# Optimization experiments

Hardware: AMD Instinct MI355X
Metric: run time of the kernel (lower is better)

## Reference

```python
import jax, jax.numpy as jnp
import numpy as np

N, R, E, DIN, DOUT, B = 40000, 16, 50000, 256, 256, 4


def setup_inputs() -> dict:
    key = jax.random.key(0)
    ks = jax.random.split(key, 7)
    xav = (2.0 / (DIN + DOUT)) ** 0.5  # xavier-ish scale
    x = jax.random.normal(ks[0], (N, DIN), jnp.float32)
    bases = jax.random.normal(ks[1], (B, DIN, DOUT), jnp.float32) * xav
    coeff = jax.random.normal(ks[2], (R, B), jnp.float32) * 0.5
    loop_weight = jax.random.normal(ks[3], (DIN, DOUT), jnp.float32) * xav
    h_bias = jnp.zeros((DOUT,), jnp.float32)
    edge_src = jax.random.randint(ks[4], (R, E), 0, N, dtype=jnp.int64)
    edge_dst = jax.random.randint(ks[5], (R, E), 0, N, dtype=jnp.int64)
    return {"x": x, "bases": bases, "coeff": coeff, "loop_weight": loop_weight,
            "h_bias": h_bias, "edge_src": edge_src, "edge_dst": edge_dst}


def reference(x, bases, coeff, loop_weight, h_bias, edge_src, edge_dst):
    # Basis decomposition: per-relation weight W_r = sum_b coeff[r,b] * bases[b]
    W = jnp.einsum('rb,bio->rio', coeff, bases)  # [R, DIN, DOUT]
    n = x.shape[0]

    def body(acc, rel):
        W_r, src, dst = rel
        # transform all nodes once, gather at edge sources
        m = (x @ W_r)[src]                                   # [E, DOUT]
        agg = jax.ops.segment_sum(m, dst, num_segments=n)    # [N, DOUT]
        deg = jax.ops.segment_sum(jnp.ones(src.shape, jnp.float32), dst,
                                  num_segments=n)            # in-degree per rel
        # norm='right': divide by dst in-degree (clamped to 1)
        return acc + agg / jnp.clip(deg, 1.0)[:, None], None

    h0 = jnp.zeros((n, loop_weight.shape[1]), x.dtype)
    h, _ = jax.lax.scan(body, h0, (W, edge_src, edge_dst))   # sum over relations
    h = h + x @ loop_weight + h_bias                         # self-loop + bias
    return jax.nn.relu(h)
```

## Files before the change

### kernel.cpp

```cpp
#include <hip/hip_runtime.h>
#include <stdint.h>

#define NN   40000
#define RR   16
#define EE   50000
#define DD   256
#define NB   4
#define KTOT (NB*DD + DD)
#define BM   128
#define BN   128
#define BK   32
#define NITER (KTOT/BK)

#define SCAN_BLK  40
#define SCAN_ELEM 1024

typedef __bf16 bf16x8 __attribute__((ext_vector_type(8)));
typedef float  f32x4  __attribute__((ext_vector_type(4)));
typedef float  f32x2  __attribute__((ext_vector_type(2)));
typedef unsigned short ushort_t;

__device__ inline unsigned short f2bf(float f) {
    unsigned int b = __builtin_bit_cast(unsigned int, f);
    b += 0x7FFFu + ((b >> 16) & 1u);
    return (unsigned short)(b >> 16);
}

__device__ __forceinline__ void gll16(const void* g, void* l) {
    __builtin_amdgcn_global_load_lds(
        (__attribute__((address_space(1))) void*)(uintptr_t)g,
        (__attribute__((address_space(3))) void*)(uint32_t)(uintptr_t)l,
        16, 0, 0);
}


#define CAST_BLKS ((NN * DD / 4 + DD * KTOT + 255) / 256)
#define DEG_BLKS  ((RR * EE + 255) / 256)

__global__ __launch_bounds__(256) void k_prep(const float* __restrict__ x,
                                              const float* __restrict__ bases,
                                              const float* __restrict__ lw,
                                              const int* __restrict__ edst,
                                              ushort_t* __restrict__ xb,
                                              ushort_t* __restrict__ Bt,
                                              int* __restrict__ deg) {
    int b = blockIdx.x;
    if (b < CAST_BLKS) {
        int t = b * 256 + threadIdx.x;
        const int NX = NN * DD / 4;
        if (t < NX) {
            float4 f = *(const float4*)(x + (size_t)t * 4);
            ushort4 o;
            o.x = f2bf(f.x); o.y = f2bf(f.y); o.z = f2bf(f.z); o.w = f2bf(f.w);
            *(ushort4*)(xb + (size_t)t * 4) = o;
        } else {
            int u = t - NX;
            if (u < DD * KTOT) {
                int o = u / KTOT, k = u - o * KTOT;
                float f = (k < NB * DD) ? bases[(size_t)k * DD + o]
                                        : lw[(size_t)(k - NB * DD) * DD + o];
                Bt[u] = f2bf(f);
            }
        }
    } else {
        int e = (b - CAST_BLKS) * 256 + threadIdx.x;
        if (e < RR * EE) {
            int r = e / EE;
            atomicAdd(&deg[r * NN + edst[e]], 1);
        }
    }
}

__global__ __launch_bounds__(256) void k_scanA(const int* __restrict__ deg,
                                               int* __restrict__ offsets,
                                               int* __restrict__ bsum) {
    __shared__ int part[256];
    int t = threadIdx.x, b = blockIdx.x;
    int g = b * SCAN_ELEM + t * 4;
    int4 h = {0, 0, 0, 0};
    if (g < NN) {
#pragma unroll
        for (int r = 0; r < RR; r++) {
            int4 d = *(const int4*)(deg + (size_t)r * NN + g);
            h.x += d.x; h.y += d.y; h.z += d.z; h.w += d.w;
        }
    }
    int s = h.x + h.y + h.z + h.w;
    part[t] = s;
    __syncthreads();
    for (int off = 1; off < 256; off <<= 1) {
        int v = (t >= off) ? part[t - off] : 0;
        __syncthreads();
        part[t] += v;
        __syncthreads();
    }
    int ex = part[t] - s;
    if (g < NN) {
        int4 o;
        o.x = ex;
        o.y = ex + h.x;
        o.z = ex + h.x + h.y;
        o.w = ex + h.x + h.y + h.z;
        *(int4*)(offsets + g) = o;
    }
    if (t == 255) bsum[b] = part[255];
}

__global__ __launch_bounds__(256) void k_scanB(const int* __restrict__ bsum,
                                               int* __restrict__ offsets,
                                               int* __restrict__ cursor) {
    __shared__ int sbase, stot;
    int t = threadIdx.x, b = blockIdx.x;
    if (t == 0) {
        int acc = 0, base = 0;
        for (int i = 0; i < SCAN_BLK; i++) {
            if (i == b) base = acc;
            acc += bsum[i];
        }
        sbase = base;
        stot = acc;
    }
    __syncthreads();
    int base = sbase;
    int g = b * SCAN_ELEM + t * 4;
    if (g < NN) {
        int4 o = *(const int4*)(offsets + g);
        o.x += base; o.y += base; o.z += base; o.w += base;
        *(int4*)(offsets + g) = o;
        *(int4*)(cursor + g) = o;
    }
    if (b == SCAN_BLK - 1 && t == 0) offsets[NN] = stot;
}

__global__ __launch_bounds__(256) void k_escatter(const int* __restrict__ esrc,
                                                  const int* __restrict__ edst,
                                                  int* __restrict__ cursor,
                                                  unsigned int* __restrict__ recs) {
    int e = blockIdx.x * blockDim.x + threadIdx.x;
    if (e >= RR * EE) return;
    int r = e / EE;
    int d = edst[e];
    int pos = atomicAdd(&cursor[d], 1);
    recs[pos] = (unsigned int)esrc[e] | ((unsigned int)r << 16);
}

__global__ __launch_bounds__(256) void k_gather(const ushort_t* __restrict__ xb,
                                                const float* __restrict__ coeff,
                                                const int* __restrict__ deg,
                                                const int* __restrict__ offsets,
                                                const unsigned int* __restrict__ recs,
                                                ushort_t* __restrict__ vb) {
    __shared__ float wtab[4][64];
    int lane = threadIdx.x & 63;
    int wv   = threadIdx.x >> 6;
    int n    = __builtin_amdgcn_readfirstlane(blockIdx.x * 4 + wv);

    {
        int r  = lane >> 2;
        int dg = deg[r * NN + n];
        float inv = 1.0f / (float)(dg > 0 ? dg : 1);
        wtab[wv][lane] = coeff[lane] * inv;
    }

    int beg = offsets[n], end = offsets[n + 1];
    f32x2 a[4][2];
#pragma unroll
    for (int b = 0; b < 4; b++) { a[b][0] = (f32x2){0,0}; a[b][1] = (f32x2){0,0}; }

    const float* wrow = &wtab[wv][0];
    const ushort_t* xl = xb + lane * 4;

    auto acc_edge = [&](uint2 u, float4 w) {
        f32x2 lo, hi;
        lo.x = __builtin_bit_cast(float, u.x << 16);
        lo.y = __builtin_bit_cast(float, u.x & 0xFFFF0000u);
        hi.x = __builtin_bit_cast(float, u.y << 16);
        hi.y = __builtin_bit_cast(float, u.y & 0xFFFF0000u);
        a[0][0] = lo * (f32x2){w.x, w.x} + a[0][0];
        a[0][1] = hi * (f32x2){w.x, w.x} + a[0][1];
        a[1][0] = lo * (f32x2){w.y, w.y} + a[1][0];
        a[1][1] = hi * (f32x2){w.y, w.y} + a[1][1];
        a[2][0] = lo * (f32x2){w.z, w.z} + a[2][0];
        a[2][1] = hi * (f32x2){w.z, w.z} + a[2][1];
        a[3][0] = lo * (f32x2){w.w, w.w} + a[3][0];
        a[3][1] = hi * (f32x2){w.w, w.w} + a[3][1];
    };

    int ei = beg;
    for (; ei + 4 <= end; ei += 4) {
        unsigned int r0 = recs[ei + 0];
        unsigned int r1 = recs[ei + 1];
        unsigned int r2 = recs[ei + 2];
        unsigned int r3 = recs[ei + 3];
        uint2 u0 = *(const uint2*)(xl + (size_t)(r0 & 0xFFFFu) * DD);
        uint2 u1 = *(const uint2*)(xl + (size_t)(r1 & 0xFFFFu) * DD);
        uint2 u2 = *(const uint2*)(xl + (size_t)(r2 & 0xFFFFu) * DD);
        uint2 u3 = *(const uint2*)(xl + (size_t)(r3 & 0xFFFFu) * DD);
        float4 w0 = *(const float4*)&wrow[(r0 >> 16) * 4];
        float4 w1 = *(const float4*)&wrow[(r1 >> 16) * 4];
        float4 w2 = *(const float4*)&wrow[(r2 >> 16) * 4];
        float4 w3 = *(const float4*)&wrow[(r3 >> 16) * 4];
        acc_edge(u0, w0);
        acc_edge(u1, w1);
        acc_edge(u2, w2);
        acc_edge(u3, w3);
    }
    for (; ei < end; ei++) {
        unsigned int r0 = recs[ei];
        uint2 u0 = *(const uint2*)(xl + (size_t)(r0 & 0xFFFFu) * DD);
        float4 w0 = *(const float4*)&wrow[(r0 >> 16) * 4];
        acc_edge(u0, w0);
    }

    ushort_t* vr = vb + (size_t)n * (NB * DD) + lane * 4;
#pragma unroll
    for (int b = 0; b < 4; b++) {
        ushort4 o;
        o.x = f2bf(a[b][0].x); o.y = f2bf(a[b][0].y);
        o.z = f2bf(a[b][1].x); o.w = f2bf(a[b][1].y);
        *(ushort4*)(vr + b * DD) = o;
    }
}

__global__ __launch_bounds__(256) void k_gemm(const ushort_t* __restrict__ vb,
                                              const ushort_t* __restrict__ xb,
                                              const ushort_t* __restrict__ Bt,
                                              const float* __restrict__ bias,
                                              float* __restrict__ out) {
    __shared__ __align__(16) ushort_t As[2][BM * BK];
    __shared__ __align__(16) ushort_t Bs[2][BN * BK];
    int tid  = threadIdx.x;
    int lane = tid & 63;
    int w    = tid >> 6;
    int wr   = w >> 1, wc = w & 1;
    int rowbase = blockIdx.y * BM;
    int nbase   = blockIdx.x * BN;
    int ml = lane & 15, q = lane >> 4;

    int srow  = tid >> 2;
    int g     = (tid & 3) ^ ((tid >> 4) & 3);
    int wbase = __builtin_amdgcn_readfirstlane(w << 10);

    int arow0 = rowbase + srow;       if (arow0 >= NN) arow0 = NN - 1;
    int arow1 = rowbase + 64 + srow;  if (arow1 >= NN) arow1 = NN - 1;
    const ushort_t* pvA0 = vb + (size_t)arow0 * (NB * DD) + g * 8;
    const ushort_t* pvA1 = vb + (size_t)arow1 * (NB * DD) + g * 8;
    const ushort_t* pxA0 = xb + (size_t)arow0 * DD + g * 8;
    const ushort_t* pxA1 = xb + (size_t)arow1 * DD + g * 8;
    const ushort_t* pB0  = Bt + (size_t)(nbase + srow) * KTOT + g * 8;
    const ushort_t* pB1  = Bt + (size_t)(nbase + 64 + srow) * KTOT + g * 8;

    f32x4 acc[4][4];
#pragma unroll
    for (int i = 0; i < 4; i++)
#pragma unroll
        for (int j = 0; j < 4; j++) acc[i][j] = (f32x4){0, 0, 0, 0};

    int aoff[4], boff[4];
#pragma unroll
    for (int i = 0; i < 4; i++) {
        int m = wr * 64 + i * 16 + ml;
        aoff[i] = m * BK + ((q ^ ((m >> 2) & 3)) * 8);
    }
#pragma unroll
    for (int j = 0; j < 4; j++) {
        int n = wc * 64 + j * 16 + ml;
        boff[j] = n * BK + ((q ^ ((n >> 2) & 3)) * 8);
    }

    auto stage = [&](int s, int kb) {
        const ushort_t* a0 = (kb < NB * DD) ? pvA0 + kb : pxA0 + (kb - NB * DD);
        const ushort_t* a1 = (kb < NB * DD) ? pvA1 + kb : pxA1 + (kb - NB * DD);
        char* ab = (char*)&As[s][0] + wbase;
        char* bb = (char*)&Bs[s][0] + wbase;
        gll16(a0,       ab);
        gll16(a1,       ab + 4096);
        gll16(pB0 + kb, bb);
        gll16(pB1 + kb, bb + 4096);
    };

    stage(0, 0);
    asm volatile("s_waitcnt vmcnt(0)" ::: "memory");
    __syncthreads();

    for (int it = 0; it < NITER; ++it) {
        int cur = it & 1;
        if (it + 1 < NITER) stage(cur ^ 1, (it + 1) * BK);
        bf16x8 af[4], bf[4];
#pragma unroll
        for (int i = 0; i < 4; i++) af[i] = *(const bf16x8*)&As[cur][aoff[i]];
#pragma unroll
        for (int j = 0; j < 4; j++) bf[j] = *(const bf16x8*)&Bs[cur][boff[j]];
#pragma unroll
        for (int i = 0; i < 4; i++)
#pragma unroll
            for (int j = 0; j < 4; j++)
                acc[i][j] = __builtin_amdgcn_mfma_f32_16x16x32_bf16(af[i], bf[j], acc[i][j], 0, 0, 0);
        asm volatile("s_waitcnt vmcnt(0)" ::: "memory");
        __syncthreads();
    }

#pragma unroll
    for (int i = 0; i < 4; i++) {
#pragma unroll
        for (int r = 0; r < 4; r++) {
            int ng = rowbase + wr * 64 + i * 16 + q * 4 + r;
            if (ng < NN) {
#pragma unroll
                for (int j = 0; j < 4; j++) {
                    int o = nbase + wc * 64 + j * 16 + ml;
                    float vv = acc[i][j][r] + bias[o];
                    out[(size_t)ng * DD + o] = fmaxf(vv, 0.0f);
                }
            }
        }
    }
}

extern "C" void kernel_launch(void* const* d_in, const int* in_sizes, int n_in,
                              void* d_out, int out_size, void* d_ws, size_t ws_size,
                              hipStream_t stream) {
    const float* x     = (const float*)d_in[0];
    const float* bases = (const float*)d_in[1];
    const float* coeff = (const float*)d_in[2];
    const float* lw    = (const float*)d_in[3];
    const float* bias  = (const float*)d_in[4];
    const int*   esrc  = (const int*)d_in[5];
    const int*   edst  = (const int*)d_in[6];
    float* out = (float*)d_out;

    char* ws = (char*)d_ws;
    ushort_t*     vb      = (ushort_t*)(ws);
    ushort_t*     xb      = (ushort_t*)(ws + 81920000);
    ushort_t*     Bt      = (ushort_t*)(ws + 102400000);
    int*          deg     = (int*)(ws + 103055360);
    int*          offsets = (int*)(ws + 105775360);
    int*          cursor  = (int*)(ws + 105935376);
    unsigned int* recs    = (unsigned int*)(ws + 106095376);
    int*          bsum    = (int*)(ws + 109295376);

    hipMemsetAsync(deg, 0, (size_t)RR * NN * sizeof(int), stream);

    int ne = RR * EE;
    k_prep<<<CAST_BLKS + DEG_BLKS, 256, 0, stream>>>(x, bases, lw, edst, xb, Bt, deg);
    k_scanA<<<SCAN_BLK, 256, 0, stream>>>(deg, offsets, bsum);
    k_scanB<<<SCAN_BLK, 256, 0, stream>>>(bsum, offsets, cursor);
    k_escatter<<<(ne + 255) / 256, 256, 0, stream>>>(esrc, edst, cursor, recs);
    k_gather<<<NN / 4, 256, 0, stream>>>(xb, coeff, deg, offsets, recs, vb);
    dim3 ggrid(DD / BN, (NN + BM - 1) / BM);
    k_gemm<<<ggrid, 256, 0, stream>>>(vb, xb, Bt, bias, out);
}
```

Before: 288.2 us.

## Transpose degree array to node-major and make gather kernel grid-stride persistent

The per-relation degree array is stored node-major ([N][R]) instead of relation-major, so the scan reads 16 contiguous ints per node and the gather reads one contiguous 64-byte row. The gather kernel now launches a fixed 2048 blocks that loop over nodes in grid-stride fashion, with coeff loaded once per lane and launch bounds requesting higher occupancy. This cuts launch/block-scheduling overhead and strided degree reads. The risk is worse load balance across waves, since each wave now handles several nodes with uneven edge counts.

```diff
diff --git a/kernel.cpp b/kernel.cpp
--- a/kernel.cpp
+++ b/kernel.cpp
@@ -14,6 +14,9 @@
 
 #define SCAN_BLK  40
 #define SCAN_ELEM 1024
+
+#define GATHER_BLKS 2048
+#define NWAVES (GATHER_BLKS * 4)
 
 typedef __bf16 bf16x8 __attribute__((ext_vector_type(8)));
 typedef float  f32x4  __attribute__((ext_vector_type(4)));
@@ -66,7 +69,7 @@
         int e = (b - CAST_BLKS) * 256 + threadIdx.x;
         if (e < RR * EE) {
             int r = e / EE;
-            atomicAdd(&deg[r * NN + edst[e]], 1);
+            atomicAdd(&deg[(size_t)edst[e] * RR + r], 1);
         }
     }
 }
@@ -77,15 +80,17 @@
     __shared__ int part[256];
     int t = threadIdx.x, b = blockIdx.x;
     int g = b * SCAN_ELEM + t * 4;
-    int4 h = {0, 0, 0, 0};
+    int hh[4] = {0, 0, 0, 0};
     if (g < NN) {
 #pragma unroll
-        for (int r = 0; r < RR; r++) {
-            int4 d = *(const int4*)(deg + (size_t)r * NN + g);
-            h.x += d.x; h.y += d.y; h.z += d.z; h.w += d.w;
-        }
-    }
-    int s = h.x + h.y + h.z + h.w;
+        for (int i = 0; i < 4; i++) {
+            const int4* dp = (const int4*)(deg + (size_t)(g + i) * RR);
+            int4 d0 = dp[0], d1 = dp[1], d2 = dp[2], d3 = dp[3];
+            hh[i] = d0.x + d0.y + d0.z + d0.w + d1.x + d1.y + d1.z + d1.w
+                  + d2.x + d2.y + d2.z + d2.w + d3.x + d3.y + d3.z + d3.w;
+        }
+    }
+    int s = hh[0] + hh[1] + hh[2] + hh[3];
     part[t] = s;
     __syncthreads();
     for (int off = 1; off < 256; off <<= 1) {
@@ -98,9 +103,9 @@
     if (g < NN) {
         int4 o;
         o.x = ex;
-        o.y = ex + h.x;
-        o.z = ex + h.x + h.y;
-        o.w = ex + h.x + h.y + h.z;
+        o.y = ex + hh[0];
+        o.z = ex + hh[0] + hh[1];
+        o.w = ex + hh[0] + hh[1] + hh[2];
         *(int4*)(offsets + g) = o;
     }
     if (t == 255) bsum[b] = part[255];
@@ -144,81 +149,84 @@
     recs[pos] = (unsigned int)esrc[e] | ((unsigned int)r << 16);
 }
 
-__global__ __launch_bounds__(256) void k_gather(const ushort_t* __restrict__ xb,
-                                                const float* __restrict__ coeff,
-                                                const int* __restrict__ deg,
-                                                const int* __restrict__ offsets,
-                                                const unsigned int* __restrict__ recs,
-                                                ushort_t* __restrict__ vb) {
+__global__ __launch_bounds__(256, 8) void k_gather(const ushort_t* __restrict__ xb,
+                                                   const float* __restrict__ coeff,
+                                                   const int* __restrict__ deg,
+                                                   const int* __restrict__ offsets,
+                                                   const unsigned int* __restrict__ recs,
+                                                   ushort_t* __restrict__ vb) {
     __shared__ float wtab[4][64];
     int lane = threadIdx.x & 63;
     int wv   = threadIdx.x >> 6;
-    int n    = __builtin_amdgcn_readfirstlane(blockIdx.x * 4 + wv);
-
-    {
-        int r  = lane >> 2;
-        int dg = deg[r * NN + n];
-        float inv = 1.0f / (float)(dg > 0 ? dg : 1);
-        wtab[wv][lane] = coeff[lane] * inv;
-    }
-
-    int beg = offsets[n], end = offsets[n + 1];
-    f32x2 a[4][2];
-#pragma unroll
-    for (int b = 0; b < 4; b++) { a[b][0] = (f32x2){0,0}; a[b][1] = (f32x2){0,0}; }
-
+    int gw   = __builtin_amdgcn_readfirstlane(blockIdx.x * 4 + wv);
+
+    const ushort_t* xl = xb + lane * 4;
     const float* wrow = &wtab[wv][0];
-    const ushort_t* xl = xb + lane * 4;
-
-    auto acc_edge = [&](uint2 u, float4 w) {
-        f32x2 lo, hi;
-        lo.x = __builtin_bit_cast(float, u.x << 16);
-        lo.y = __builtin_bit_cast(float, u.x & 0xFFFF0000u);
-        hi.x = __builtin_bit_cast(float, u.y << 16);
-        hi.y = __builtin_bit_cast(float, u.y & 0xFFFF0000u);
-        a[0][0] = lo * (f32x2){w.x, w.x} + a[0][0];
-        a[0][1] = hi * (f32x2){w.x, w.x} + a[0][1];
-        a[1][0] = lo * (f32x2){w.y, w.y} + a[1][0];
-        a[1][1] = hi * (f32x2){w.y, w.y} + a[1][1];
-        a[2][0] = lo * (f32x2){w.z, w.z} + a[2][0];
-        a[2][1] = hi * (f32x2){w.z, w.z} + a[2][1];
-        a[3][0] = lo * (f32x2){w.w, w.w} + a[3][0];
-        a[3][1] = hi * (f32x2){w.w, w.w} + a[3][1];
-    };
-
-    int ei = beg;
-    for (; ei + 4 <= end; ei += 4) {
-        unsigned int r0 = recs[ei + 0];
-        unsigned int r1 = recs[ei + 1];
-        unsigned int r2 = recs[ei + 2];
-        unsigned int r3 = recs[ei + 3];
-        uint2 u0 = *(const uint2*)(xl + (size_t)(r0 & 0xFFFFu) * DD);
-        uint2 u1 = *(const uint2*)(xl + (size_t)(r1 & 0xFFFFu) * DD);
-        uint2 u2 = *(const uint2*)(xl + (size_t)(r2 & 0xFFFFu) * DD);
-        uint2 u3 = *(const uint2*)(xl + (size_t)(r3 & 0xFFFFu) * DD);
-        float4 w0 = *(const float4*)&wrow[(r0 >> 16) * 4];
-        float4 w1 = *(const float4*)&wrow[(r1 >> 16) * 4];
-        float4 w2 = *(const float4*)&wrow[(r2 >> 16) * 4];
-        float4 w3 = *(const float4*)&wrow[(r3 >> 16) * 4];
-        acc_edge(u0, w0);
-        acc_edge(u1, w1);
-        acc_edge(u2, w2);
-        acc_edge(u3, w3);
-    }
-    for (; ei < end; ei++) {
-        unsigned int r0 = recs[ei];
-        uint2 u0 = *(const uint2*)(xl + (size_t)(r0 & 0xFFFFu) * DD);
-        float4 w0 = *(const float4*)&wrow[(r0 >> 16) * 4];
-        acc_edge(u0, w0);
-    }
-
-    ushort_t* vr = vb + (size_t)n * (NB * DD) + lane * 4;
-#pragma unroll
-    for (int b = 0; b < 4; b++) {
-        ushort4 o;
-        o.x = f2bf(a[b][0].x); o.y = f2bf(a[b][0].y);
-        o.z = f2bf(a[b][1].x); o.w = f2bf(a[b][1].y);
-        *(ushort4*)(vr + b * DD) = o;
+    float cf = coeff[lane];
+    int rsel = lane >> 2;
+
+    for (int n = gw; n < NN; n += NWAVES) {
+        {
+            int dg = deg[(size_t)n * RR + rsel];
+            float inv = 1.0f / (float)(dg > 0 ? dg : 1);
+            wtab[wv][lane] = cf * inv;
+        }
+
+        int beg = offsets[n], end = offsets[n + 1];
+        f32x2 a[4][2];
+#pragma unroll
+        for (int b = 0; b < 4; b++) { a[b][0] = (f32x2){0,0}; a[b][1] = (f32x2){0,0}; }
+
+        auto acc_edge = [&](uint2 u, float4 w) {
+            f32x2 lo, hi;
+            lo.x = __builtin_bit_cast(float, u.x << 16);
+            lo.y = __builtin_bit_cast(float, u.x & 0xFFFF0000u);
+            hi.x = __builtin_bit_cast(float, u.y << 16);
+            hi.y = __builtin_bit_cast(float, u.y & 0xFFFF0000u);
+            a[0][0] = lo * (f32x2){w.x, w.x} + a[0][0];
+            a[0][1] = hi * (f32x2){w.x, w.x} + a[0][1];
+            a[1][0] = lo * (f32x2){w.y, w.y} + a[1][0];
+            a[1][1] = hi * (f32x2){w.y, w.y} + a[1][1];
+            a[2][0] = lo * (f32x2){w.z, w.z} + a[2][0];
+            a[2][1] = hi * (f32x2){w.z, w.z} + a[2][1];
+            a[3][0] = lo * (f32x2){w.w, w.w} + a[3][0];
+            a[3][1] = hi * (f32x2){w.w, w.w} + a[3][1];
+        };
+
+        int ei = beg;
+        for (; ei + 4 <= end; ei += 4) {
+            unsigned int r0 = recs[ei + 0];
+            unsigned int r1 = recs[ei + 1];
+            unsigned int r2 = recs[ei + 2];
+            unsigned int r3 = recs[ei + 3];
+            uint2 u0 = *(const uint2*)(xl + (size_t)(r0 & 0xFFFFu) * DD);
+            uint2 u1 = *(const uint2*)(xl + (size_t)(r1 & 0xFFFFu) * DD);
+            uint2 u2 = *(const uint2*)(xl + (size_t)(r2 & 0xFFFFu) * DD);
+            uint2 u3 = *(const uint2*)(xl + (size_t)(r3 & 0xFFFFu) * DD);
+            float4 w0 = *(const float4*)&wrow[(r0 >> 16) * 4];
+            float4 w1 = *(const float4*)&wrow[(r1 >> 16) * 4];
+            float4 w2 = *(const float4*)&wrow[(r2 >> 16) * 4];
+            float4 w3 = *(const float4*)&wrow[(r3 >> 16) * 4];
+            acc_edge(u0, w0);
+            acc_edge(u1, w1);
+            acc_edge(u2, w2);
+            acc_edge(u3, w3);
+        }
+        for (; ei < end; ei++) {
+            unsigned int r0 = recs[ei];
+            uint2 u0 = *(const uint2*)(xl + (size_t)(r0 & 0xFFFFu) * DD);
+            float4 w0 = *(const float4*)&wrow[(r0 >> 16) * 4];
+            acc_edge(u0, w0);
+        }
+
+        ushort_t* vr = vb + (size_t)n * (NB * DD) + lane * 4;
+#pragma unroll
+        for (int b = 0; b < 4; b++) {
+            ushort4 o;
+            o.x = f2bf(a[b][0].x); o.y = f2bf(a[b][0].y);
+            o.z = f2bf(a[b][1].x); o.w = f2bf(a[b][1].y);
+            *(ushort4*)(vr + b * DD) = o;
+        }
     }
 }
 
@@ -346,7 +354,7 @@
     k_scanA<<<SCAN_BLK, 256, 0, stream>>>(deg, offsets, bsum);
     k_scanB<<<SCAN_BLK, 256, 0, stream>>>(bsum, offsets, cursor);
     k_escatter<<<(ne + 255) / 256, 256, 0, stream>>>(esrc, edst, cursor, recs);
-    k_gather<<<NN / 4, 256, 0, stream>>>(xb, coeff, deg, offsets, recs, vb);
+    k_gather<<<GATHER_BLKS, 256, 0, stream>>>(xb, coeff, deg, offsets, recs, vb);
     dim3 ggrid(DD / BN, (NN + BM - 1) / BM);
     k_gemm<<<ggrid, 256, 0, stream>>>(vb, xb, Bt, bias, out);
 }
```

Result: no change. 291.9 us (+1.3%).
